# Kernel optimization log

Hardware: AMD Instinct MI355X
Metric: run time of the kernel (lower is better)

Reference implementation:

```python
import jax, jax.numpy as jnp
import numpy as np


def _gru_cell(x, h, Wih, Whh):
    # PyTorch GRU (bias=False): gates ordered [r, z, n] along rows of W.
    gi = x @ Wih.T              # [B, 3H]
    gh = h @ Whh.T              # [B, 3H]
    ir, iz, inn = jnp.split(gi, 3, axis=-1)
    hr, hz, hn = jnp.split(gh, 3, axis=-1)
    r = jax.nn.sigmoid(ir + hr)
    z = jax.nn.sigmoid(iz + hz)
    n = jnp.tanh(inn + r * hn)
    return (1.0 - z) * n + z * h


def setup_inputs() -> dict:
    key = jax.random.key(0)
    ks = jax.random.split(key, 16)
    B, T = 256, 1024
    U, Z, Y, H = 16, 16, 16, 128
    W = 0.1  # weight scale for stable recurrence
    inp = {
        "u": jax.random.normal(ks[0], (B, U, T), jnp.float32),
        "y": jax.random.normal(ks[1], (B, Y, T), jnp.float32),
        "h0": jax.random.uniform(ks[2], (2, B, H), jnp.float32),
        "Wih0": W * jax.random.normal(ks[3], (3 * H, U + Z), jnp.float32),
        "Whh0": W * jax.random.normal(ks[4], (3 * H, H), jnp.float32),
        "Wih1": W * jax.random.normal(ks[5], (3 * H, H), jnp.float32),
        "Whh1": W * jax.random.normal(ks[6], (3 * H, H), jnp.float32),
        "dW1": W * jax.random.normal(ks[7], (H, U + H), jnp.float32),
        "db1": jnp.zeros((H,), jnp.float32),
        "dW2": W * jax.random.normal(ks[8], (Z, H), jnp.float32),
        "db2": jnp.zeros((Z,), jnp.float32),
        "mW1": W * jax.random.normal(ks[9], (H, Z + H), jnp.float32),
        "mb1": jnp.zeros((H,), jnp.float32),
        "mW2": W * jax.random.normal(ks[10], (H, H), jnp.float32),
        "mb2": jnp.zeros((H,), jnp.float32),
        "mW3": W * jax.random.normal(ks[11], (Y, H), jnp.float32),
        "mb3": jnp.zeros((Y,), jnp.float32),
    }
    return inp


def reference(u, y, h0, Wih0, Whh0, Wih1, Whh1,
              dW1, db1, dW2, db2, mW1, mb1, mW2, mb2, mW3, mb3):
    B, Z = u.shape[0], dW2.shape[0]
    u_t = jnp.transpose(u, (2, 0, 1))  # [T, B, U]
    y_t = jnp.transpose(y, (2, 0, 1))  # [T, B, Y]

    def step(carry, xs):
        h, x_prev, loss = carry  # h: [2, B, H]
        ut, yt = xs
        inp = jnp.concatenate([ut, x_prev], axis=1)       # [B, U+Z]
        h0n = _gru_cell(inp, h[0], Wih0, Whh0)
        h1n = _gru_cell(h0n, h[1], Wih1, Whh1)
        h_new = jnp.stack([h0n, h1n], axis=0)
        # dynn: two Linears, no activation; input cat(u_t, h[-1])
        d_in = jnp.concatenate([ut, h1n], axis=1)         # [B, U+H]
        x_t = (d_in @ dW1.T + db1) @ dW2.T + db2          # [B, Z]
        # menn: Linear -> ReLU -> Linear -> Linear; input cat(x_t, h[0])
        m_in = jnp.concatenate([x_t, h0n], axis=1)        # [B, Z+H]
        m = jax.nn.relu(m_in @ mW1.T + mb1)
        m = m @ mW2.T + mb2
        y_hat = m @ mW3.T + mb3                           # [B, Y]
        loss = loss + jnp.sum((y_hat - yt) ** 2)
        return (h_new, x_t, loss), None

    x0 = jnp.zeros((B, Z), jnp.float32)  # x_tm1 at t=0 is zeros
    (_, _, loss), _ = jax.lax.scan(step, (h0, x0, jnp.float32(0.0)), (u_t, y_t))
    return loss
```

## Files before the change

### kernel.cpp

```cpp
#include <hip/hip_runtime.h>

typedef __bf16 bf16x8 __attribute__((ext_vector_type(8)));
typedef float f32x4 __attribute__((ext_vector_type(4)));
typedef unsigned int uint32;
typedef unsigned short u16;

#define T_STEPS 1024

#define H0_OFF   0
#define H1_OFF   8704
#define M1_OFF   17408
#define UCH_OFF  21760
#define YCH_OFF  46336
#define WL_OFF   70912
#define LDS_BYTES 145664

#define TG0 0
#define TG1 24
#define TG2 120
#define TG3 216
#define TG4 312
#define TG5 317
#define TG6 357
#define NT_TOT 361
#define SC_DC  369664
#define SC_ME  378880
#define SC_DBC 387072
#define SC_MBE 387136

static __device__ __forceinline__ u16 f2bf(float f) {
    uint32 u = __builtin_bit_cast(uint32, f);
    return (u16)((u + 0x7FFFu + ((u >> 16) & 1u)) >> 16);
}
static __device__ __forceinline__ float bf2f(u16 h) {
    uint32 u = ((uint32)h) << 16;
    return __builtin_bit_cast(float, u);
}
static __device__ __forceinline__ uint32 cvtpk(float a, float b) {
    uint32 r;
    asm("v_cvt_pk_bf16_f32 %0, %1, %2" : "=v"(r) : "v"(a), "v"(b));
    return r;
}
static __device__ __forceinline__ float sigm(float x) {
    return __builtin_amdgcn_rcpf(1.f + __builtin_amdgcn_exp2f(x * -1.4426950408889634f));
}
static __device__ __forceinline__ float tanh_fast(float x) {
    float xm = fmaxf(x, -30.f);
    float e = __builtin_amdgcn_exp2f(xm * -2.8853900817779268f);
    return fmaf(2.f, __builtin_amdgcn_rcpf(e + 1.f), -1.f);
}
static __device__ __forceinline__ f32x4 mfma16(bf16x8 a, bf16x8 b, f32x4 c) {
    return __builtin_amdgcn_mfma_f32_16x16x32_bf16(a, b, c, 0, 0, 0);
}
static __device__ __forceinline__ bf16x8 ldsAF(const char* p) {
    return __builtin_bit_cast(bf16x8, *(const uint4*)p);
}

__global__ void prep1(const float* __restrict__ dW1, const float* __restrict__ db1,
                      const float* __restrict__ dW2, const float* __restrict__ db2,
                      const float* __restrict__ mW2, const float* __restrict__ mb2,
                      const float* __restrict__ mW3, const float* __restrict__ mb3,
                      char* __restrict__ ws, float* __restrict__ out) {
    int id = blockIdx.x * 256 + threadIdx.x;
    if (id == 0) *out = 0.f;
    if (id < 2304) {
        int n = id / 144, k = id % 144;
        float s = 0.f;
        for (int h = 0; h < 128; ++h) s += dW2[n * 128 + h] * dW1[h * 144 + k];
        ((float*)(ws + SC_DC))[id] = s;
    } else if (id < 4352) {
        int e = id - 2304, n = e / 128, k = e % 128;
        float s = 0.f;
        for (int h = 0; h < 128; ++h) s += mW3[n * 128 + h] * mW2[h * 128 + k];
        ((float*)(ws + SC_ME))[e] = s;
    } else if (id < 4368) {
        int n = id - 4352;
        float s = db2[n];
        for (int h = 0; h < 128; ++h) s += dW2[n * 128 + h] * db1[h];
        ((float*)(ws + SC_DBC))[n] = s;
    } else if (id < 4384) {
        int n = id - 4368;
        float s = mb3[n];
        for (int h = 0; h < 128; ++h) s += mW3[n * 128 + h] * mb2[h];
        ((float*)(ws + SC_MBE))[n] = s;
    }
}

__global__ void prep2(const float* __restrict__ W0, const float* __restrict__ W1,
                      const float* __restrict__ W2, const float* __restrict__ W3,
                      const float* __restrict__ W5, char* __restrict__ ws) {
    const int tt = blockIdx.x;
    const int lane = threadIdx.x;
    const int cum[8] = {TG0, TG1, TG2, TG3, TG4, TG5, TG6, NT_TOT};
    const int Kreal[7] = {32, 128, 128, 128, 144, 144, 128};
    const int KT[7] = {1, 4, 4, 4, 5, 5, 4};
    const float* Ws[7] = {W0, W1, W2, W3, (const float*)(ws + SC_DC), W5, (const float*)(ws + SC_ME)};
    int g = 0;
    while (tt >= cum[g + 1]) ++g;
    const int tl = tt - cum[g];
    const int kt = tl % KT[g];
    const int n = (tl / KT[g]) * 16 + (lane & 15);
    const float* W = Ws[g];
    u16* o = (u16*)ws + tt * 512 + lane * 8;
#pragma unroll
    for (int j = 0; j < 8; ++j) {
        int k = kt * 32 + (lane >> 4) * 8 + j;
        o[j] = (k < Kreal[g]) ? f2bf(W[n * Kreal[g] + k]) : (u16)0;
    }
}

__global__ __launch_bounds__(512, 2) void rnn_main(
    const float* __restrict__ u, const float* __restrict__ yg, const float* __restrict__ h0g,
    const char* __restrict__ ws, const float* __restrict__ mb1g,
    const float* __restrict__ dbCg, const float* __restrict__ mbEg,
    float* __restrict__ out) {
    __shared__ __align__(16) char smem[LDS_BYTES];
    const int tid = threadIdx.x;
    const int lane = tid & 63;
    const int w = tid >> 6;
    const int lr = lane & 15;
    const int lg = lane >> 4;
    const int r0 = blockIdx.x * 16;
    const uint4* F4 = (const uint4*)ws;
    const f32x4 zero = {0.f, 0.f, 0.f, 0.f};
    const bf16x8 z8 = __builtin_bit_cast(bf16x8, (uint4){0u, 0u, 0u, 0u});

    for (int i = tid; i < 1024; i += 512) {
        int lay = i >> 9, rem = i & 511, rr = rem >> 5, k4 = rem & 31;
        float4 v = *(const float4*)(h0g + (lay * 256 + r0 + rr) * 128 + k4 * 4);
        uint2 pk;
        pk.x = (uint32)f2bf(v.x) | ((uint32)f2bf(v.y) << 16);
        pk.y = (uint32)f2bf(v.z) | ((uint32)f2bf(v.w) << 16);
        *(uint2*)(smem + H0_OFF + lay * 8704 + rr * 272 + k4 * 8) = pk;
    }
    for (int i = tid; i < 73 * 64; i += 512) {
        int li = i >> 6, ln2 = i & 63;
        int gt2 = (li < 24) ? li : (li < 29) ? TG4 + (li - 24) : (li < 69) ? TG5 + (li - 29) : TG6 + (li - 69);
        *((uint4*)(smem + WL_OFF) + i) = F4[gt2 * 64 + ln2];
    }
    __syncthreads();

    bf16x8 wW[3][3][4];
    for (int p = 0; p < 6; ++p) {
        for (int i = tid; i < 3072; i += 512)
            *((uint4*)(smem + UCH_OFF) + i) = F4[(TG1 + p * 48) * 64 + i];
        __syncthreads();
#pragma unroll
        for (int mat = 0; mat < 3; ++mat)
#pragma unroll
            for (int gg = 0; gg < 3; ++gg) {
                int rel0 = mat * 96 + gg * 32 + w * 4;
                if (rel0 >= p * 48 && rel0 < p * 48 + 48) {
#pragma unroll
                    for (int kt = 0; kt < 4; ++kt)
                        wW[mat][gg][kt] = ldsAF(smem + UCH_OFF + (rel0 - p * 48 + kt) * 1024 + lane * 16);
                }
            }
        __syncthreads();
    }

    const float mb1_c = mb1g[w * 16 + lr];
    const float mbE_l = mbEg[lr];
    float dbc4[4];
#pragma unroll
    for (int i = 0; i < 4; ++i) dbc4[i] = dbCg[lg * 4 + i];
    float hp0[4], hp1[4];
#pragma unroll
    for (int i = 0; i < 4; ++i) {
        hp0[i] = h0g[(r0 + lg * 4 + i) * 128 + w * 16 + lr];
        hp1[i] = h0g[(256 + r0 + lg * 4 + i) * 128 + w * 16 + lr];
    }
    float loss = 0.f;
    const int c2 = (w * 16 + lr) * 2;
    const int bp0 = (lr + (lg & 1) * 32) * 4;

    for (int t = 0; t < T_STEPS; ++t) {
        const char* h0c = smem + H0_OFF + (t & 1) * 4352;
        char* h0n = smem + H0_OFF + ((t & 1) ^ 1) * 4352;
        const char* h1c = smem + H1_OFF + (t & 1) * 4352;
        char* h1n = smem + H1_OFF + ((t & 1) ^ 1) * 4352;
        const int s = t & 31, sp = (t - 1) & 31;

        const char* h1r = h1c + lr * 272;
        bf16x8 ad0 = ldsAF((lg < 2) ? (smem + UCH_OFF + sp * 768 + lr * 48 + lg * 16)
                                    : (h1r + (lg - 2) * 16));
        bf16x8 ad1 = ldsAF(h1r + 32 + lg * 16);
        bf16x8 ad2 = ldsAF(h1r + 96 + lg * 16);
        bf16x8 ad3 = ldsAF(h1r + 160 + lg * 16);
        bf16x8 ad4t = ldsAF(h1r + 224 + (lg & 1) * 16);
        bf16x8 ad4 = (lg < 2) ? ad4t : z8;
        f32x4 xa = mfma16(ldsAF(smem + WL_OFF + 24 * 1024 + lane * 16), ad0, zero);
        xa = mfma16(ldsAF(smem + WL_OFF + 25 * 1024 + lane * 16), ad1, xa);
        xa = mfma16(ldsAF(smem + WL_OFF + 26 * 1024 + lane * 16), ad2, xa);
        f32x4 xb = mfma16(ldsAF(smem + WL_OFF + 27 * 1024 + lane * 16), ad3, zero);
        xb = mfma16(ldsAF(smem + WL_OFF + 28 * 1024 + lane * 16), ad4, xb);
        uint32 pk0 = cvtpk(xa[0] + xb[0] + dbc4[0], xa[1] + xb[1] + dbc4[1]);
        uint32 pk1 = cvtpk(xa[2] + xb[2] + dbc4[2], xa[3] + xb[3] + dbc4[3]);
        if (t == 0) { pk0 = 0u; pk1 = 0u; }
        uint32 d0 = (uint32)__builtin_amdgcn_ds_bpermute(bp0, (int)pk0);
        uint32 d1 = (uint32)__builtin_amdgcn_ds_bpermute(bp0, (int)pk1);
        uint32 d2 = (uint32)__builtin_amdgcn_ds_bpermute(bp0 + 64, (int)pk0);
        uint32 d3 = (uint32)__builtin_amdgcn_ds_bpermute(bp0 + 64, (int)pk1);
        bf16x8 xfrag = __builtin_bit_cast(bf16x8, (uint4){d0, d1, d2, d3});

        if ((t & 31) == 0) {
            __syncthreads();
            for (int q = 0; q < 16; ++q) {
                int pair = w * 32 + q * 2 + (lane >> 5);
                int rr2 = pair >> 4, ch = pair & 15, ss = lane & 31;
                float v = u[(r0 + rr2) * 16384 + ch * 1024 + t + ss];
                *(u16*)(smem + UCH_OFF + ss * 768 + rr2 * 48 + ch * 2) = f2bf(v);
            }
            for (int q = 0; q < 16; ++q) {
                int pair = w * 32 + q * 2 + (lane >> 5);
                int rr2 = pair >> 4, ch = pair & 15, ss = lane & 31;
                int gt = t - 1 + ss;
                if (gt >= 0 && gt < T_STEPS) {
                    float v = yg[(r0 + rr2) * 16384 + ch * 1024 + gt];
                    *(u16*)(smem + YCH_OFF + ss * 768 + rr2 * 48 + ch * 2) = f2bf(v);
                }
            }
            __syncthreads();
        }

        bf16x8 ufrag = ldsAF(smem + UCH_OFF + s * 768 + lr * 48 + (lg & 1) * 16);
        bf16x8 a_inp = (lg < 2) ? ufrag : xfrag;
        const char* h0r = h0c + lr * 272;
        bf16x8 ah0 = ldsAF(h0r + lg * 16);
        bf16x8 ah1 = ldsAF(h0r + 64 + lg * 16);
        bf16x8 ah2 = ldsAF(h0r + 128 + lg * 16);
        bf16x8 ah3 = ldsAF(h0r + 192 + lg * 16);
        bf16x8 b0r = ldsAF(smem + WL_OFF + (0 * 8 + w) * 1024 + lane * 16);
        bf16x8 b0z = ldsAF(smem + WL_OFF + (1 * 8 + w) * 1024 + lane * 16);
        bf16x8 b0n = ldsAF(smem + WL_OFF + (2 * 8 + w) * 1024 + lane * 16);
        f32x4 rA = mfma16(ah0, wW[0][0][0], zero);
        rA = mfma16(ah1, wW[0][0][1], rA);
        rA = mfma16(a_inp, b0r, rA);
        f32x4 rB = mfma16(ah2, wW[0][0][2], zero);
        rB = mfma16(ah3, wW[0][0][3], rB);
        f32x4 zA = mfma16(ah0, wW[0][1][0], zero);
        zA = mfma16(ah1, wW[0][1][1], zA);
        zA = mfma16(a_inp, b0z, zA);
        f32x4 zB = mfma16(ah2, wW[0][1][2], zero);
        zB = mfma16(ah3, wW[0][1][3], zB);
        f32x4 nI = mfma16(a_inp, b0n, zero);
        f32x4 nA = mfma16(ah0, wW[0][2][0], zero);
        nA = mfma16(ah1, wW[0][2][1], nA);
        f32x4 nB = mfma16(ah2, wW[0][2][2], zero);
        nB = mfma16(ah3, wW[0][2][3], nB);
        bf16x8 t0 = ldsAF(h0r + (lg & 1) * 16);
        bf16x8 am0 = (lg < 2) ? xfrag : t0;
        bf16x8 am1 = ldsAF(h0r + 32 + lg * 16);
        bf16x8 am2 = ldsAF(h0r + 96 + lg * 16);
        bf16x8 am3 = ldsAF(h0r + 160 + lg * 16);
        bf16x8 am4t = ldsAF(h0r + 224 + (lg & 1) * 16);
        bf16x8 am4 = (lg < 2) ? am4t : z8;
        f32x4 mA = mfma16(am1, ldsAF(smem + WL_OFF + (29 + w * 5 + 1) * 1024 + lane * 16), zero);
        mA = mfma16(am2, ldsAF(smem + WL_OFF + (29 + w * 5 + 2) * 1024 + lane * 16), mA);
        mA = mfma16(am0, ldsAF(smem + WL_OFF + (29 + w * 5 + 0) * 1024 + lane * 16), mA);
        f32x4 mB = mfma16(am3, ldsAF(smem + WL_OFF + (29 + w * 5 + 3) * 1024 + lane * 16), zero);
        mB = mfma16(am4, ldsAF(smem + WL_OFF + (29 + w * 5 + 4) * 1024 + lane * 16), mB);
#pragma unroll
        for (int i = 0; i < 4; ++i) {
            float rr = sigm(rA[i] + rB[i]);
            float zz = sigm(zA[i] + zB[i]);
            float nn = tanh_fast(fmaf(rr, nA[i] + nB[i], nI[i]));
            float hnew = fmaf(zz, hp0[i] - nn, nn);
            hp0[i] = hnew;
            *(u16*)(h0n + (lg * 4 + i) * 272 + c2) = (u16)cvtpk(hnew, hnew);
            float mv = fmaxf(mA[i] + mB[i] + mb1_c, 0.f);
            *(u16*)(smem + M1_OFF + (lg * 4 + i) * 272 + c2) = (u16)cvtpk(mv, mv);
        }
        __syncthreads();

        const char* h0nr = h0n + lr * 272;
        bf16x8 ag0 = ldsAF(h0nr + lg * 16);
        bf16x8 ag1 = ldsAF(h0nr + 64 + lg * 16);
        bf16x8 ag2 = ldsAF(h0nr + 128 + lg * 16);
        bf16x8 ag3 = ldsAF(h0nr + 192 + lg * 16);
        bf16x8 av0 = ldsAF(h1r + lg * 16);
        bf16x8 av1 = ldsAF(h1r + 64 + lg * 16);
        bf16x8 av2 = ldsAF(h1r + 128 + lg * 16);
        bf16x8 av3 = ldsAF(h1r + 192 + lg * 16);
        f32x4 RA = mfma16(ag0, wW[1][0][0], zero);
        RA = mfma16(ag1, wW[1][0][1], RA);
        RA = mfma16(ag2, wW[1][0][2], RA);
        RA = mfma16(ag3, wW[1][0][3], RA);
        f32x4 RB = mfma16(av0, wW[2][0][0], zero);
        RB = mfma16(av1, wW[2][0][1], RB);
        RB = mfma16(av2, wW[2][0][2], RB);
        RB = mfma16(av3, wW[2][0][3], RB);
        f32x4 ZA = mfma16(ag0, wW[1][1][0], zero);
        ZA = mfma16(ag1, wW[1][1][1], ZA);
        ZA = mfma16(ag2, wW[1][1][2], ZA);
        ZA = mfma16(ag3, wW[1][1][3], ZA);
        f32x4 ZB = mfma16(av0, wW[2][1][0], zero);
        ZB = mfma16(av1, wW[2][1][1], ZB);
        ZB = mfma16(av2, wW[2][1][2], ZB);
        ZB = mfma16(av3, wW[2][1][3], ZB);
        f32x4 NI = mfma16(ag0, wW[1][2][0], zero);
        NI = mfma16(ag1, wW[1][2][1], NI);
        NI = mfma16(ag2, wW[1][2][2], NI);
        NI = mfma16(ag3, wW[1][2][3], NI);
        f32x4 NH = mfma16(av0, wW[2][2][0], zero);
        NH = mfma16(av1, wW[2][2][1], NH);
        NH = mfma16(av2, wW[2][2][2], NH);
        NH = mfma16(av3, wW[2][2][3], NH);
#pragma unroll
        for (int i = 0; i < 4; ++i) {
            float rr = sigm(RA[i] + RB[i]);
            float zz = sigm(ZA[i] + ZB[i]);
            float nn = tanh_fast(fmaf(rr, NH[i], NI[i]));
            float hnew = fmaf(zz, hp1[i] - nn, nn);
            hp1[i] = hnew;
            *(u16*)(h1n + (lg * 4 + i) * 272 + c2) = (u16)cvtpk(hnew, hnew);
        }
        if (w == 7) {
            const char* m1r = smem + M1_OFF + lr * 272;
            bf16x8 q0 = ldsAF(m1r + lg * 16);
            bf16x8 q1 = ldsAF(m1r + 64 + lg * 16);
            bf16x8 q2 = ldsAF(m1r + 128 + lg * 16);
            bf16x8 q3 = ldsAF(m1r + 192 + lg * 16);
            f32x4 lA = mfma16(q0, ldsAF(smem + WL_OFF + 69 * 1024 + lane * 16), zero);
            lA = mfma16(q1, ldsAF(smem + WL_OFF + 70 * 1024 + lane * 16), lA);
            f32x4 lB = mfma16(q2, ldsAF(smem + WL_OFF + 71 * 1024 + lane * 16), zero);
            lB = mfma16(q3, ldsAF(smem + WL_OFF + 72 * 1024 + lane * 16), lB);
            const float gd = (t > 0) ? 1.f : 0.f;
#pragma unroll
            for (int i = 0; i < 4; ++i) {
                float yh = lA[i] + lB[i] + mbE_l;
                float yv = bf2f(*(const u16*)(smem + YCH_OFF + s * 768 + (lg * 4 + i) * 48 + lr * 2));
                float d = yh - yv;
                loss = fmaf(gd * d, d, loss);
            }
        }
        __syncthreads();
    }

    {
        const char* h0c = smem + H0_OFF;
        const char* h1c = smem + H1_OFF;
        const char* h1r = h1c + lr * 272;
        const char* h0r = h0c + lr * 272;
        bf16x8 ad0 = ldsAF((lg < 2) ? (smem + UCH_OFF + 31 * 768 + lr * 48 + lg * 16)
                                    : (h1r + (lg - 2) * 16));
        bf16x8 ad1 = ldsAF(h1r + 32 + lg * 16);
        bf16x8 ad2 = ldsAF(h1r + 96 + lg * 16);
        bf16x8 ad3 = ldsAF(h1r + 160 + lg * 16);
        bf16x8 ad4t = ldsAF(h1r + 224 + (lg & 1) * 16);
        bf16x8 ad4 = (lg < 2) ? ad4t : z8;
        f32x4 xa = mfma16(ldsAF(smem + WL_OFF + 24 * 1024 + lane * 16), ad0, zero);
        xa = mfma16(ldsAF(smem + WL_OFF + 25 * 1024 + lane * 16), ad1, xa);
        xa = mfma16(ldsAF(smem + WL_OFF + 26 * 1024 + lane * 16), ad2, xa);
        f32x4 xb = mfma16(ldsAF(smem + WL_OFF + 27 * 1024 + lane * 16), ad3, zero);
        xb = mfma16(ldsAF(smem + WL_OFF + 28 * 1024 + lane * 16), ad4, xb);
        uint32 pk0 = cvtpk(xa[0] + xb[0] + dbc4[0], xa[1] + xb[1] + dbc4[1]);
        uint32 pk1 = cvtpk(xa[2] + xb[2] + dbc4[2], xa[3] + xb[3] + dbc4[3]);
        uint32 d0 = (uint32)__builtin_amdgcn_ds_bpermute(bp0, (int)pk0);
        uint32 d1 = (uint32)__builtin_amdgcn_ds_bpermute(bp0, (int)pk1);
        uint32 d2 = (uint32)__builtin_amdgcn_ds_bpermute(bp0 + 64, (int)pk0);
        uint32 d3 = (uint32)__builtin_amdgcn_ds_bpermute(bp0 + 64, (int)pk1);
        bf16x8 xfrag = __builtin_bit_cast(bf16x8, (uint4){d0, d1, d2, d3});
        bf16x8 t0 = ldsAF(h0r + (lg & 1) * 16);
        bf16x8 am0 = (lg < 2) ? xfrag : t0;
        bf16x8 am1 = ldsAF(h0r + 32 + lg * 16);
        bf16x8 am2 = ldsAF(h0r + 96 + lg * 16);
        bf16x8 am3 = ldsAF(h0r + 160 + lg * 16);
        bf16x8 am4t = ldsAF(h0r + 224 + (lg & 1) * 16);
        bf16x8 am4 = (lg < 2) ? am4t : z8;
        f32x4 mA = mfma16(am0, ldsAF(smem + WL_OFF + (29 + w * 5 + 0) * 1024 + lane * 16), zero);
        mA = mfma16(am1, ldsAF(smem + WL_OFF + (29 + w * 5 + 1) * 1024 + lane * 16), mA);
        mA = mfma16(am2, ldsAF(smem + WL_OFF + (29 + w * 5 + 2) * 1024 + lane * 16), mA);
        f32x4 mB = mfma16(am3, ldsAF(smem + WL_OFF + (29 + w * 5 + 3) * 1024 + lane * 16), zero);
        mB = mfma16(am4, ldsAF(smem + WL_OFF + (29 + w * 5 + 4) * 1024 + lane * 16), mB);
#pragma unroll
        for (int i = 0; i < 4; ++i) {
            float mv = fmaxf(mA[i] + mB[i] + mb1_c, 0.f);
            *(u16*)(smem + M1_OFF + (lg * 4 + i) * 272 + c2) = (u16)cvtpk(mv, mv);
        }
        __syncthreads();
        if (w == 7) {
            const char* m1r = smem + M1_OFF + lr * 272;
            bf16x8 q0 = ldsAF(m1r + lg * 16);
            bf16x8 q1 = ldsAF(m1r + 64 + lg * 16);
            bf16x8 q2 = ldsAF(m1r + 128 + lg * 16);
            bf16x8 q3 = ldsAF(m1r + 192 + lg * 16);
            f32x4 lA = mfma16(q0, ldsAF(smem + WL_OFF + 69 * 1024 + lane * 16), zero);
            lA = mfma16(q1, ldsAF(smem + WL_OFF + 70 * 1024 + lane * 16), lA);
            f32x4 lB = mfma16(q2, ldsAF(smem + WL_OFF + 71 * 1024 + lane * 16), zero);
            lB = mfma16(q3, ldsAF(smem + WL_OFF + 72 * 1024 + lane * 16), lB);
#pragma unroll
            for (int i = 0; i < 4; ++i) {
                float yh = lA[i] + lB[i] + mbE_l;
                float yv = yg[(r0 + lg * 4 + i) * 16384 + lr * 1024 + 1023];
                float d = yh - yv;
                loss = fmaf(d, d, loss);
            }
        }
    }

    if (w == 7) {
#pragma unroll
        for (int off = 32; off > 0; off >>= 1) loss += __shfl_down(loss, off, 64);
        if (lane == 0) atomicAdd(out, loss);
    }
}

extern "C" void kernel_launch(void* const* d_in, const int* in_sizes, int n_in,
                              void* d_out, int out_size, void* d_ws, size_t ws_size,
                              hipStream_t stream) {
    const float* u    = (const float*)d_in[0];
    const float* y    = (const float*)d_in[1];
    const float* h0   = (const float*)d_in[2];
    const float* Wih0 = (const float*)d_in[3];
    const float* Whh0 = (const float*)d_in[4];
    const float* Wih1 = (const float*)d_in[5];
    const float* Whh1 = (const float*)d_in[6];
    const float* dW1  = (const float*)d_in[7];
    const float* db1  = (const float*)d_in[8];
    const float* dW2  = (const float*)d_in[9];
    const float* db2  = (const float*)d_in[10];
    const float* mW1  = (const float*)d_in[11];
    const float* mb1  = (const float*)d_in[12];
    const float* mW2  = (const float*)d_in[13];
    const float* mb2  = (const float*)d_in[14];
    const float* mW3  = (const float*)d_in[15];
    const float* mb3  = (const float*)d_in[16];
    float* out = (float*)d_out;
    char* ws = (char*)d_ws;

    prep1<<<dim3(18), dim3(256), 0, stream>>>(dW1, db1, dW2, db2, mW2, mb2, mW3, mb3, ws, out);
    prep2<<<dim3(NT_TOT), dim3(64), 0, stream>>>(Wih0, Whh0, Wih1, Whh1, mW1, ws);
    rnn_main<<<dim3(16), dim3(512), 0, stream>>>(u, y, h0, ws, mb1,
                                                 (const float*)(ws + SC_DBC),
                                                 (const float*)(ws + SC_MBE), out);
}
```

Baseline: 2.778 ms.

## Halve workgroup to four waves, each computing two column tiles of the GRU

Shrinks the block from 8 waves to 4. Each wave now owns two 16-column tiles, so it holds twice as many weight fragments in registers, runs twice the MFMAs and has more independent accumulator chains. It also prefetches the hidden-state fragments across the step boundary, merges the u and y chunk loads, pads the chunk stride to reduce LDS bank conflicts, and drops the zero-select masking. The aim is cheaper barriers and better MFMA pipelining on this latency-bound recurrence. The cost is higher register pressure and half as many waves to hide latency.

```diff
diff --git a/kernel.cpp b/kernel.cpp
--- a/kernel.cpp
+++ b/kernel.cpp
@@ -11,9 +11,10 @@
 #define H1_OFF   8704
 #define M1_OFF   17408
 #define UCH_OFF  21760
-#define YCH_OFF  46336
-#define WL_OFF   70912
-#define LDS_BYTES 145664
+#define YCH_OFF  46848
+#define WL_OFF   71936
+#define LDS_BYTES 146688
+#define CH_STR   784
 
 #define TG0 0
 #define TG1 24
@@ -109,7 +110,7 @@
     }
 }
 
-__global__ __launch_bounds__(512, 2) void rnn_main(
+__global__ __launch_bounds__(256, 1) void rnn_main(
     const float* __restrict__ u, const float* __restrict__ yg, const float* __restrict__ h0g,
     const char* __restrict__ ws, const float* __restrict__ mb1g,
     const float* __restrict__ dbCg, const float* __restrict__ mbEg,
@@ -123,9 +124,8 @@
     const int r0 = blockIdx.x * 16;
     const uint4* F4 = (const uint4*)ws;
     const f32x4 zero = {0.f, 0.f, 0.f, 0.f};
-    const bf16x8 z8 = __builtin_bit_cast(bf16x8, (uint4){0u, 0u, 0u, 0u});
-
-    for (int i = tid; i < 1024; i += 512) {
+
+    for (int i = tid; i < 1024; i += 256) {
         int lay = i >> 9, rem = i & 511, rr = rem >> 5, k4 = rem & 31;
         float4 v = *(const float4*)(h0g + (lay * 256 + r0 + rr) * 128 + k4 * 4);
         uint2 pk;
@@ -133,67 +133,93 @@
         pk.y = (uint32)f2bf(v.z) | ((uint32)f2bf(v.w) << 16);
         *(uint2*)(smem + H0_OFF + lay * 8704 + rr * 272 + k4 * 8) = pk;
     }
-    for (int i = tid; i < 73 * 64; i += 512) {
+    for (int i = tid; i < 73 * 64; i += 256) {
         int li = i >> 6, ln2 = i & 63;
         int gt2 = (li < 24) ? li : (li < 29) ? TG4 + (li - 24) : (li < 69) ? TG5 + (li - 29) : TG6 + (li - 69);
         *((uint4*)(smem + WL_OFF) + i) = F4[gt2 * 64 + ln2];
     }
     __syncthreads();
 
-    bf16x8 wW[3][3][4];
+    bf16x8 wW[3][3][2][4];
     for (int p = 0; p < 6; ++p) {
-        for (int i = tid; i < 3072; i += 512)
+        for (int i = tid; i < 3072; i += 256)
             *((uint4*)(smem + UCH_OFF) + i) = F4[(TG1 + p * 48) * 64 + i];
         __syncthreads();
 #pragma unroll
         for (int mat = 0; mat < 3; ++mat)
 #pragma unroll
-            for (int gg = 0; gg < 3; ++gg) {
-                int rel0 = mat * 96 + gg * 32 + w * 4;
-                if (rel0 >= p * 48 && rel0 < p * 48 + 48) {
-#pragma unroll
-                    for (int kt = 0; kt < 4; ++kt)
-                        wW[mat][gg][kt] = ldsAF(smem + UCH_OFF + (rel0 - p * 48 + kt) * 1024 + lane * 16);
+            for (int gg = 0; gg < 3; ++gg)
+#pragma unroll
+                for (int j = 0; j < 2; ++j) {
+                    int rel0 = mat * 96 + gg * 32 + (2 * w + j) * 4;
+                    if (rel0 >= p * 48 && rel0 < p * 48 + 48) {
+#pragma unroll
+                        for (int kt = 0; kt < 4; ++kt)
+                            wW[mat][gg][j][kt] =
+                                ldsAF(smem + UCH_OFF + (rel0 - p * 48 + kt) * 1024 + lane * 16);
+                    }
                 }
-            }
         __syncthreads();
     }
 
-    const float mb1_c = mb1g[w * 16 + lr];
+    float mb1_c[2] = {mb1g[w * 32 + lr], mb1g[w * 32 + 16 + lr]};
     const float mbE_l = mbEg[lr];
     float dbc4[4];
 #pragma unroll
     for (int i = 0; i < 4; ++i) dbc4[i] = dbCg[lg * 4 + i];
-    float hp0[4], hp1[4];
-#pragma unroll
-    for (int i = 0; i < 4; ++i) {
-        hp0[i] = h0g[(r0 + lg * 4 + i) * 128 + w * 16 + lr];
-        hp1[i] = h0g[(256 + r0 + lg * 4 + i) * 128 + w * 16 + lr];
-    }
+    float hp0[2][4], hp1[2][4];
+#pragma unroll
+    for (int j = 0; j < 2; ++j)
+#pragma unroll
+        for (int i = 0; i < 4; ++i) {
+            hp0[j][i] = h0g[(r0 + lg * 4 + i) * 128 + w * 32 + j * 16 + lr];
+            hp1[j][i] = h0g[(256 + r0 + lg * 4 + i) * 128 + w * 32 + j * 16 + lr];
+        }
     float loss = 0.f;
-    const int c2 = (w * 16 + lr) * 2;
     const int bp0 = (lr + (lg & 1) * 32) * 4;
 
+    bf16x8 pf_ah[4];
+#pragma unroll
+    for (int kt = 0; kt < 4; ++kt) pf_ah[kt] = ldsAF(smem + H0_OFF + lr * 272 + kt * 64 + lg * 16);
+
+#pragma unroll 2
     for (int t = 0; t < T_STEPS; ++t) {
         const char* h0c = smem + H0_OFF + (t & 1) * 4352;
         char* h0n = smem + H0_OFF + ((t & 1) ^ 1) * 4352;
         const char* h1c = smem + H1_OFF + (t & 1) * 4352;
         char* h1n = smem + H1_OFF + ((t & 1) ^ 1) * 4352;
         const int s = t & 31, sp = (t - 1) & 31;
-
         const char* h1r = h1c + lr * 272;
-        bf16x8 ad0 = ldsAF((lg < 2) ? (smem + UCH_OFF + sp * 768 + lr * 48 + lg * 16)
+
+        bf16x8 ad0 = ldsAF((lg < 2) ? (smem + UCH_OFF + sp * CH_STR + lr * 48 + lg * 16)
                                     : (h1r + (lg - 2) * 16));
         bf16x8 ad1 = ldsAF(h1r + 32 + lg * 16);
         bf16x8 ad2 = ldsAF(h1r + 96 + lg * 16);
         bf16x8 ad3 = ldsAF(h1r + 160 + lg * 16);
-        bf16x8 ad4t = ldsAF(h1r + 224 + (lg & 1) * 16);
-        bf16x8 ad4 = (lg < 2) ? ad4t : z8;
-        f32x4 xa = mfma16(ldsAF(smem + WL_OFF + 24 * 1024 + lane * 16), ad0, zero);
-        xa = mfma16(ldsAF(smem + WL_OFF + 25 * 1024 + lane * 16), ad1, xa);
-        xa = mfma16(ldsAF(smem + WL_OFF + 26 * 1024 + lane * 16), ad2, xa);
-        f32x4 xb = mfma16(ldsAF(smem + WL_OFF + 27 * 1024 + lane * 16), ad3, zero);
-        xb = mfma16(ldsAF(smem + WL_OFF + 28 * 1024 + lane * 16), ad4, xb);
+        bf16x8 ad4 = ldsAF(h1r + 224 + (lg & 1) * 16);
+        bf16x8 wd0 = ldsAF(smem + WL_OFF + 24 * 1024 + lane * 16);
+        bf16x8 wd1 = ldsAF(smem + WL_OFF + 25 * 1024 + lane * 16);
+        bf16x8 wd2 = ldsAF(smem + WL_OFF + 26 * 1024 + lane * 16);
+        bf16x8 wd3 = ldsAF(smem + WL_OFF + 27 * 1024 + lane * 16);
+        bf16x8 wd4 = ldsAF(smem + WL_OFF + 28 * 1024 + lane * 16);
+
+        f32x4 hR[2], hZ[2], hN[2], nI[2];
+#pragma unroll
+        for (int j = 0; j < 2; ++j) { hR[j] = zero; hZ[j] = zero; hN[j] = zero; }
+#pragma unroll
+        for (int kt = 0; kt < 4; ++kt)
+#pragma unroll
+            for (int j = 0; j < 2; ++j) {
+                hR[j] = mfma16(pf_ah[kt], wW[0][0][j][kt], hR[j]);
+                hZ[j] = mfma16(pf_ah[kt], wW[0][1][j][kt], hZ[j]);
+                hN[j] = mfma16(pf_ah[kt], wW[0][2][j][kt], hN[j]);
+            }
+
+        f32x4 xa = mfma16(wd0, ad0, zero);
+        xa = mfma16(wd1, ad1, xa);
+        xa = mfma16(wd2, ad2, xa);
+        f32x4 xb = mfma16(wd3, ad3, zero);
+        xb = mfma16(wd4, ad4, xb);
         uint32 pk0 = cvtpk(xa[0] + xb[0] + dbc4[0], xa[1] + xb[1] + dbc4[1]);
         uint32 pk1 = cvtpk(xa[2] + xb[2] + dbc4[2], xa[3] + xb[3] + dbc4[3]);
         if (t == 0) { pk0 = 0u; pk1 = 0u; }
@@ -205,135 +231,131 @@
 
         if ((t & 31) == 0) {
             __syncthreads();
-            for (int q = 0; q < 16; ++q) {
-                int pair = w * 32 + q * 2 + (lane >> 5);
+            for (int q = 0; q < 32; ++q) {
+                int pair = w * 64 + q * 2 + (lane >> 5);
                 int rr2 = pair >> 4, ch = pair & 15, ss = lane & 31;
                 float v = u[(r0 + rr2) * 16384 + ch * 1024 + t + ss];
-                *(u16*)(smem + UCH_OFF + ss * 768 + rr2 * 48 + ch * 2) = f2bf(v);
-            }
-            for (int q = 0; q < 16; ++q) {
-                int pair = w * 32 + q * 2 + (lane >> 5);
-                int rr2 = pair >> 4, ch = pair & 15, ss = lane & 31;
+                *(u16*)(smem + UCH_OFF + ss * CH_STR + rr2 * 48 + ch * 2) = f2bf(v);
                 int gt = t - 1 + ss;
-                if (gt >= 0 && gt < T_STEPS) {
-                    float v = yg[(r0 + rr2) * 16384 + ch * 1024 + gt];
-                    *(u16*)(smem + YCH_OFF + ss * 768 + rr2 * 48 + ch * 2) = f2bf(v);
+                if (gt >= 0) {
+                    float vy = yg[(r0 + rr2) * 16384 + ch * 1024 + gt];
+                    *(u16*)(smem + YCH_OFF + ss * CH_STR + rr2 * 48 + ch * 2) = f2bf(vy);
                 }
             }
             __syncthreads();
         }
 
-        bf16x8 ufrag = ldsAF(smem + UCH_OFF + s * 768 + lr * 48 + (lg & 1) * 16);
+        bf16x8 ufrag = ldsAF(smem + UCH_OFF + s * CH_STR + lr * 48 + (lg & 1) * 16);
         bf16x8 a_inp = (lg < 2) ? ufrag : xfrag;
+#pragma unroll
+        for (int j = 0; j < 2; ++j) {
+            bf16x8 b0r = ldsAF(smem + WL_OFF + (0 * 8 + 2 * w + j) * 1024 + lane * 16);
+            bf16x8 b0z = ldsAF(smem + WL_OFF + (1 * 8 + 2 * w + j) * 1024 + lane * 16);
+            bf16x8 b0n = ldsAF(smem + WL_OFF + (2 * 8 + 2 * w + j) * 1024 + lane * 16);
+            hR[j] = mfma16(a_inp, b0r, hR[j]);
+            hZ[j] = mfma16(a_inp, b0z, hZ[j]);
+            nI[j] = mfma16(a_inp, b0n, zero);
+        }
         const char* h0r = h0c + lr * 272;
-        bf16x8 ah0 = ldsAF(h0r + lg * 16);
-        bf16x8 ah1 = ldsAF(h0r + 64 + lg * 16);
-        bf16x8 ah2 = ldsAF(h0r + 128 + lg * 16);
-        bf16x8 ah3 = ldsAF(h0r + 192 + lg * 16);
-        bf16x8 b0r = ldsAF(smem + WL_OFF + (0 * 8 + w) * 1024 + lane * 16);
-        bf16x8 b0z = ldsAF(smem + WL_OFF + (1 * 8 + w) * 1024 + lane * 16);
-        bf16x8 b0n = ldsAF(smem + WL_OFF + (2 * 8 + w) * 1024 + lane * 16);
-        f32x4 rA = mfma16(ah0, wW[0][0][0], zero);
-        rA = mfma16(ah1, wW[0][0][1], rA);
-        rA = mfma16(a_inp, b0r, rA);
-        f32x4 rB = mfma16(ah2, wW[0][0][2], zero);
-        rB = mfma16(ah3, wW[0][0][3], rB);
-        f32x4 zA = mfma16(ah0, wW[0][1][0], zero);
-        zA = mfma16(ah1, wW[0][1][1], zA);
-        zA = mfma16(a_inp, b0z, zA);
-        f32x4 zB = mfma16(ah2, wW[0][1][2], zero);
-        zB = mfma16(ah3, wW[0][1][3], zB);
-        f32x4 nI = mfma16(a_inp, b0n, zero);
-        f32x4 nA = mfma16(ah0, wW[0][2][0], zero);
-        nA = mfma16(ah1, wW[0][2][1], nA);
-        f32x4 nB = mfma16(ah2, wW[0][2][2], zero);
-        nB = mfma16(ah3, wW[0][2][3], nB);
-        bf16x8 t0 = ldsAF(h0r + (lg & 1) * 16);
-        bf16x8 am0 = (lg < 2) ? xfrag : t0;
+        bf16x8 am0 = (lg < 2) ? xfrag : ldsAF(h0r + (lg - 2) * 16);
         bf16x8 am1 = ldsAF(h0r + 32 + lg * 16);
         bf16x8 am2 = ldsAF(h0r + 96 + lg * 16);
         bf16x8 am3 = ldsAF(h0r + 160 + lg * 16);
-        bf16x8 am4t = ldsAF(h0r + 224 + (lg & 1) * 16);
-        bf16x8 am4 = (lg < 2) ? am4t : z8;
-        f32x4 mA = mfma16(am1, ldsAF(smem + WL_OFF + (29 + w * 5 + 1) * 1024 + lane * 16), zero);
-        mA = mfma16(am2, ldsAF(smem + WL_OFF + (29 + w * 5 + 2) * 1024 + lane * 16), mA);
-        mA = mfma16(am0, ldsAF(smem + WL_OFF + (29 + w * 5 + 0) * 1024 + lane * 16), mA);
-        f32x4 mB = mfma16(am3, ldsAF(smem + WL_OFF + (29 + w * 5 + 3) * 1024 + lane * 16), zero);
-        mB = mfma16(am4, ldsAF(smem + WL_OFF + (29 + w * 5 + 4) * 1024 + lane * 16), mB);
-#pragma unroll
-        for (int i = 0; i < 4; ++i) {
-            float rr = sigm(rA[i] + rB[i]);
-            float zz = sigm(zA[i] + zB[i]);
-            float nn = tanh_fast(fmaf(rr, nA[i] + nB[i], nI[i]));
-            float hnew = fmaf(zz, hp0[i] - nn, nn);
-            hp0[i] = hnew;
-            *(u16*)(h0n + (lg * 4 + i) * 272 + c2) = (u16)cvtpk(hnew, hnew);
-            float mv = fmaxf(mA[i] + mB[i] + mb1_c, 0.f);
-            *(u16*)(smem + M1_OFF + (lg * 4 + i) * 272 + c2) = (u16)cvtpk(mv, mv);
-        }
+        bf16x8 am4 = ldsAF(h0r + 224 + (lg & 1) * 16);
+        f32x4 m[2];
+#pragma unroll
+        for (int j = 0; j < 2; ++j) {
+            const int mb = 29 + (2 * w + j) * 5;
+            m[j] = mfma16(am1, ldsAF(smem + WL_OFF + (mb + 1) * 1024 + lane * 16), zero);
+            m[j] = mfma16(am2, ldsAF(smem + WL_OFF + (mb + 2) * 1024 + lane * 16), m[j]);
+            m[j] = mfma16(am0, ldsAF(smem + WL_OFF + (mb + 0) * 1024 + lane * 16), m[j]);
+            m[j] = mfma16(am3, ldsAF(smem + WL_OFF + (mb + 3) * 1024 + lane * 16), m[j]);
+            m[j] = mfma16(am4, ldsAF(smem + WL_OFF + (mb + 4) * 1024 + lane * 16), m[j]);
+        }
+#pragma unroll
+        for (int j = 0; j < 2; ++j) {
+            const int c2 = (w * 32 + j * 16 + lr) * 2;
+#pragma unroll
+            for (int i = 0; i < 4; ++i) {
+                float rr = sigm(hR[j][i]);
+                float zz = sigm(hZ[j][i]);
+                float nn = tanh_fast(fmaf(rr, hN[j][i], nI[j][i]));
+                float hnew = fmaf(zz, hp0[j][i] - nn, nn);
+                hp0[j][i] = hnew;
+                *(u16*)(h0n + (lg * 4 + i) * 272 + c2) = (u16)cvtpk(hnew, hnew);
+                float mv = fmaxf(m[j][i] + mb1_c[j], 0.f);
+                *(u16*)(smem + M1_OFF + (lg * 4 + i) * 272 + c2) = (u16)cvtpk(mv, mv);
+            }
+        }
+        bf16x8 pf_av[4];
+#pragma unroll
+        for (int kt = 0; kt < 4; ++kt) pf_av[kt] = ldsAF(h1r + kt * 64 + lg * 16);
         __syncthreads();
 
         const char* h0nr = h0n + lr * 272;
-        bf16x8 ag0 = ldsAF(h0nr + lg * 16);
-        bf16x8 ag1 = ldsAF(h0nr + 64 + lg * 16);
-        bf16x8 ag2 = ldsAF(h0nr + 128 + lg * 16);
-        bf16x8 ag3 = ldsAF(h0nr + 192 + lg * 16);
-        bf16x8 av0 = ldsAF(h1r + lg * 16);
-        bf16x8 av1 = ldsAF(h1r + 64 + lg * 16);
-        bf16x8 av2 = ldsAF(h1r + 128 + lg * 16);
-        bf16x8 av3 = ldsAF(h1r + 192 + lg * 16);
-        f32x4 RA = mfma16(ag0, wW[1][0][0], zero);
-        RA = mfma16(ag1, wW[1][0][1], RA);
-        RA = mfma16(ag2, wW[1][0][2], RA);
-        RA = mfma16(ag3, wW[1][0][3], RA);
-        f32x4 RB = mfma16(av0, wW[2][0][0], zero);
-        RB = mfma16(av1, wW[2][0][1], RB);
-        RB = mfma16(av2, wW[2][0][2], RB);
-        RB = mfma16(av3, wW[2][0][3], RB);
-        f32x4 ZA = mfma16(ag0, wW[1][1][0], zero);
-        ZA = mfma16(ag1, wW[1][1][1], ZA);
-        ZA = mfma16(ag2, wW[1][1][2], ZA);
-        ZA = mfma16(ag3, wW[1][1][3], ZA);
-        f32x4 ZB = mfma16(av0, wW[2][1][0], zero);
-        ZB = mfma16(av1, wW[2][1][1], ZB);
-        ZB = mfma16(av2, wW[2][1][2], ZB);
-        ZB = mfma16(av3, wW[2][1][3], ZB);
-        f32x4 NI = mfma16(ag0, wW[1][2][0], zero);
-        NI = mfma16(ag1, wW[1][2][1], NI);
-        NI = mfma16(ag2, wW[1][2][2], NI);
-        NI = mfma16(ag3, wW[1][2][3], NI);
-        f32x4 NH = mfma16(av0, wW[2][2][0], zero);
-        NH = mfma16(av1, wW[2][2][1], NH);
-        NH = mfma16(av2, wW[2][2][2], NH);
-        NH = mfma16(av3, wW[2][2][3], NH);
-#pragma unroll
-        for (int i = 0; i < 4; ++i) {
-            float rr = sigm(RA[i] + RB[i]);
-            float zz = sigm(ZA[i] + ZB[i]);
-            float nn = tanh_fast(fmaf(rr, NH[i], NI[i]));
-            float hnew = fmaf(zz, hp1[i] - nn, nn);
-            hp1[i] = hnew;
-            *(u16*)(h1n + (lg * 4 + i) * 272 + c2) = (u16)cvtpk(hnew, hnew);
-        }
-        if (w == 7) {
+        bf16x8 ag[4];
+#pragma unroll
+        for (int kt = 0; kt < 4; ++kt) ag[kt] = ldsAF(h0nr + kt * 64 + lg * 16);
+        bf16x8 q0, q1, q2, q3, we0, we1, we2, we3;
+        if (w == 3) {
             const char* m1r = smem + M1_OFF + lr * 272;
-            bf16x8 q0 = ldsAF(m1r + lg * 16);
-            bf16x8 q1 = ldsAF(m1r + 64 + lg * 16);
-            bf16x8 q2 = ldsAF(m1r + 128 + lg * 16);
-            bf16x8 q3 = ldsAF(m1r + 192 + lg * 16);
-            f32x4 lA = mfma16(q0, ldsAF(smem + WL_OFF + 69 * 1024 + lane * 16), zero);
-            lA = mfma16(q1, ldsAF(smem + WL_OFF + 70 * 1024 + lane * 16), lA);
-            f32x4 lB = mfma16(q2, ldsAF(smem + WL_OFF + 71 * 1024 + lane * 16), zero);
-            lB = mfma16(q3, ldsAF(smem + WL_OFF + 72 * 1024 + lane * 16), lB);
+            q0 = ldsAF(m1r + lg * 16);
+            q1 = ldsAF(m1r + 64 + lg * 16);
+            q2 = ldsAF(m1r + 128 + lg * 16);
+            q3 = ldsAF(m1r + 192 + lg * 16);
+            we0 = ldsAF(smem + WL_OFF + 69 * 1024 + lane * 16);
+            we1 = ldsAF(smem + WL_OFF + 70 * 1024 + lane * 16);
+            we2 = ldsAF(smem + WL_OFF + 71 * 1024 + lane * 16);
+            we3 = ldsAF(smem + WL_OFF + 72 * 1024 + lane * 16);
+        }
+        f32x4 R[2], Z[2], Nh[2], Ni[2];
+#pragma unroll
+        for (int j = 0; j < 2; ++j) { R[j] = zero; Z[j] = zero; Nh[j] = zero; Ni[j] = zero; }
+#pragma unroll
+        for (int kt = 0; kt < 4; ++kt)
+#pragma unroll
+            for (int j = 0; j < 2; ++j) {
+                R[j] = mfma16(pf_av[kt], wW[2][0][j][kt], R[j]);
+                Z[j] = mfma16(pf_av[kt], wW[2][1][j][kt], Z[j]);
+                Nh[j] = mfma16(pf_av[kt], wW[2][2][j][kt], Nh[j]);
+            }
+#pragma unroll
+        for (int kt = 0; kt < 4; ++kt)
+#pragma unroll
+            for (int j = 0; j < 2; ++j) {
+                R[j] = mfma16(ag[kt], wW[1][0][j][kt], R[j]);
+                Z[j] = mfma16(ag[kt], wW[1][1][j][kt], Z[j]);
+                Ni[j] = mfma16(ag[kt], wW[1][2][j][kt], Ni[j]);
+            }
+        if (w == 3) {
+            f32x4 lA = mfma16(q0, we0, zero);
+            lA = mfma16(q1, we1, lA);
+            f32x4 lB = mfma16(q2, we2, zero);
+            lB = mfma16(q3, we3, lB);
             const float gd = (t > 0) ? 1.f : 0.f;
 #pragma unroll
             for (int i = 0; i < 4; ++i) {
                 float yh = lA[i] + lB[i] + mbE_l;
-                float yv = bf2f(*(const u16*)(smem + YCH_OFF + s * 768 + (lg * 4 + i) * 48 + lr * 2));
+                float yv = bf2f(*(const u16*)(smem + YCH_OFF + s * CH_STR + (lg * 4 + i) * 48 + lr * 2));
                 float d = yh - yv;
                 loss = fmaf(gd * d, d, loss);
             }
         }
+#pragma unroll
+        for (int j = 0; j < 2; ++j) {
+            const int c2 = (w * 32 + j * 16 + lr) * 2;
+#pragma unroll
+            for (int i = 0; i < 4; ++i) {
+                float rr = sigm(R[j][i]);
+                float zz = sigm(Z[j][i]);
+                float nn = tanh_fast(fmaf(rr, Nh[j][i], Ni[j][i]));
+                float hnew = fmaf(zz, hp1[j][i] - nn, nn);
+                hp1[j][i] = hnew;
+                *(u16*)(h1n + (lg * 4 + i) * 272 + c2) = (u16)cvtpk(hnew, hnew);
+            }
+        }
+#pragma unroll
+        for (int kt = 0; kt < 4; ++kt) pf_ah[kt] = ag[kt];
         __syncthreads();
     }
 
@@ -342,13 +364,12 @@
         const char* h1c = smem + H1_OFF;
         const char* h1r = h1c + lr * 272;
         const char* h0r = h0c + lr * 272;
-        bf16x8 ad0 = ldsAF((lg < 2) ? (smem + UCH_OFF + 31 * 768 + lr * 48 + lg * 16)
+        bf16x8 ad0 = ldsAF((lg < 2) ? (smem + UCH_OFF + 31 * CH_STR + lr * 48 + lg * 16)
                                     : (h1r + (lg - 2) * 16));
         bf16x8 ad1 = ldsAF(h1r + 32 + lg * 16);
         bf16x8 ad2 = ldsAF(h1r + 96 + lg * 16);
         bf16x8 ad3 = ldsAF(h1r + 160 + lg * 16);
-        bf16x8 ad4t = ldsAF(h1r + 224 + (lg & 1) * 16);
-        bf16x8 ad4 = (lg < 2) ? ad4t : z8;
+        bf16x8 ad4 = ldsAF(h1r + 224 + (lg & 1) * 16);
         f32x4 xa = mfma16(ldsAF(smem + WL_OFF + 24 * 1024 + lane * 16), ad0, zero);
         xa = mfma16(ldsAF(smem + WL_OFF + 25 * 1024 + lane * 16), ad1, xa);
         xa = mfma16(ldsAF(smem + WL_OFF + 26 * 1024 + lane * 16), ad2, xa);
@@ -361,25 +382,28 @@
         uint32 d2 = (uint32)__builtin_amdgcn_ds_bpermute(bp0 + 64, (int)pk0);
         uint32 d3 = (uint32)__builtin_amdgcn_ds_bpermute(bp0 + 64, (int)pk1);
         bf16x8 xfrag = __builtin_bit_cast(bf16x8, (uint4){d0, d1, d2, d3});
-        bf16x8 t0 = ldsAF(h0r + (lg & 1) * 16);
-        bf16x8 am0 = (lg < 2) ? xfrag : t0;
+        bf16x8 am0 = (lg < 2) ? xfrag : ldsAF(h0r + (lg - 2) * 16);
         bf16x8 am1 = ldsAF(h0r + 32 + lg * 16);
         bf16x8 am2 = ldsAF(h0r + 96 + lg * 16);
         bf16x8 am3 = ldsAF(h0r + 160 + lg * 16);
-        bf16x8 am4t = ldsAF(h0r + 224 + (lg & 1) * 16);
-        bf16x8 am4 = (lg < 2) ? am4t : z8;
-        f32x4 mA = mfma16(am0, ldsAF(smem + WL_OFF + (29 + w * 5 + 0) * 1024 + lane * 16), zero);
-        mA = mfma16(am1, ldsAF(smem + WL_OFF + (29 + w * 5 + 1) * 1024 + lane * 16), mA);
-        mA = mfma16(am2, ldsAF(smem + WL_OFF + (29 + w * 5 + 2) * 1024 + lane * 16), mA);
-        f32x4 mB = mfma16(am3, ldsAF(smem + WL_OFF + (29 + w * 5 + 3) * 1024 + lane * 16), zero);
-        mB = mfma16(am4, ldsAF(smem + WL_OFF + (29 + w * 5 + 4) * 1024 + lane * 16), mB);
-#pragma unroll
-        for (int i = 0; i < 4; ++i) {
-            float mv = fmaxf(mA[i] + mB[i] + mb1_c, 0.f);
-            *(u16*)(smem + M1_OFF + (lg * 4 + i) * 272 + c2) = (u16)cvtpk(mv, mv);
+        bf16x8 am4 = ldsAF(h0r + 224 + (lg & 1) * 16);
+#pragma unroll
+        for (int j = 0; j < 2; ++j) {
+            const int mb = 29 + (2 * w + j) * 5;
+            f32x4 m = mfma16(am0, ldsAF(smem + WL_OFF + (mb + 0) * 1024 + lane * 16), zero);
+            m = mfma16(am1, ldsAF(smem + WL_OFF + (mb + 1) * 1024 + lane * 16), m);
+            m = mfma16(am2, ldsAF(smem + WL_OFF + (mb + 2) * 1024 + lane * 16), m);
+            m = mfma16(am3, ldsAF(smem + WL_OFF + (mb + 3) * 1024 + lane * 16), m);
+            m = mfma16(am4, ldsAF(smem + WL_OFF + (mb + 4) * 1024 + lane * 16), m);
+            const int c2 = (w * 32 + j * 16 + lr) * 2;
+#pragma unroll
+            for (int i = 0; i < 4; ++i) {
+                float mv = fmaxf(m[i] + mb1_c[j], 0.f);
+                *(u16*)(smem + M1_OFF + (lg * 4 + i) * 272 + c2) = (u16)cvtpk(mv, mv);
+            }
         }
         __syncthreads();
-        if (w == 7) {
+        if (w == 3) {
             const char* m1r = smem + M1_OFF + lr * 272;
             bf16x8 q0 = ldsAF(m1r + lg * 16);
             bf16x8 q1 = ldsAF(m1r + 64 + lg * 16);
@@ -399,7 +423,7 @@
         }
     }
 
-    if (w == 7) {
+    if (w == 3) {
 #pragma unroll
         for (int off = 32; off > 0; off >>= 1) loss += __shfl_down(loss, off, 64);
         if (lane == 0) atomicAdd(out, loss);
@@ -431,7 +455,7 @@
 
     prep1<<<dim3(18), dim3(256), 0, stream>>>(dW1, db1, dW2, db2, mW2, mb2, mW3, mb3, ws, out);
     prep2<<<dim3(NT_TOT), dim3(64), 0, stream>>>(Wih0, Whh0, Wih1, Whh1, mW1, ws);
-    rnn_main<<<dim3(16), dim3(512), 0, stream>>>(u, y, h0, ws, mb1,
+    rnn_main<<<dim3(16), dim3(256), 0, stream>>>(u, y, h0, ws, mb1,
                                                  (const float*)(ws + SC_DBC),
                                                  (const float*)(ws + SC_MBE), out);
 }
```

New measurement: 3.118 ms. 12.2% more time.
